# Kernel tuning notes

Measured on AMD Instinct MI355X. Metric: run time of the kernel, lower is better.

Reference implementation:

```python
import jax, jax.numpy as jnp
import numpy as np

D_MODEL = 1024
N_HEADS = 16
D_K = D_MODEL // N_HEADS
SEQ = 2048
BATCH = 2
THETA = 10000.0


def apply_rope(x, positions, theta):
    # x: [..., h, s, d_k], positions: [s]
    d_k = x.shape[-1]
    inv_freq = 1.0 / (theta ** (jnp.arange(0, d_k, 2, dtype=jnp.float32) / d_k))  # [d_k/2]
    ang = positions.astype(jnp.float32)[:, None] * inv_freq[None, :]  # [s, d_k/2]
    cos, sin = jnp.cos(ang), jnp.sin(ang)
    xe, xo = x[..., 0::2], x[..., 1::2]
    re = xe * cos - xo * sin
    ro = xe * sin + xo * cos
    return jnp.stack([re, ro], axis=-1).reshape(x.shape)


def setup_inputs() -> dict:
    key = jax.random.key(0)
    ks = jax.random.split(key, 7)
    f = lambda k, s: jax.random.normal(k, s, dtype=jnp.float32)
    return {
        "Q": f(ks[0], (BATCH, SEQ, D_MODEL)),
        "K": f(ks[1], (BATCH, SEQ, D_MODEL)),
        "V": f(ks[2], (BATCH, SEQ, D_MODEL)),
        "w_q": f(ks[3], (D_MODEL, D_MODEL)) * 0.02,
        "w_k": f(ks[4], (D_MODEL, D_MODEL)) * 0.02,
        "w_v": f(ks[5], (D_MODEL, D_MODEL)) * 0.02,
        "w_o": f(ks[6], (D_MODEL, D_MODEL)) * 0.02,
        "mask": jnp.tril(jnp.ones((SEQ, SEQ), dtype=bool)),
        "token_positions": jnp.arange(SEQ, dtype=jnp.int32),
    }


def reference(Q, K, V, w_q, w_k, w_v, w_o, mask, token_positions):
    h, d_k = N_HEADS, D_K
    # projections: weight is [h*d_k, d_model], applied as x @ W^T
    def proj(x, w):
        y = jnp.einsum('bsd,ed->bse', x, w)
        b, s, _ = y.shape
        return y.reshape(b, s, h, d_k).transpose(0, 2, 1, 3)  # [b,h,s,d_k]
    q = proj(Q, w_q)
    k = proj(K, w_k)
    v = proj(V, w_v)
    q = apply_rope(q, token_positions, THETA)
    k = apply_rope(k, token_positions, THETA)
    scores = jnp.einsum('bhqd,bhkd->bhqk', q, k) / jnp.sqrt(jnp.float32(d_k))
    scores = jnp.where(mask, scores, -jnp.inf)
    attn = jax.nn.softmax(scores, axis=-1)
    out = jnp.einsum('bhqk,bhkd->bhqd', attn, v)
    b, _, s, _ = out.shape
    out = out.transpose(0, 2, 1, 3).reshape(b, s, h * d_k)
    return jnp.einsum('bse,de->bsd', out, w_o)
```

## Files before the change

### kernel.cpp

```cpp
#include <hip/hip_runtime.h>

#define SEQ 2048
#define BATCH 2
#define DM 1024
#define NH 16
#define DK 64
#define BH (BATCH*NH)

typedef __attribute__((ext_vector_type(8))) short bf16x8;
typedef __attribute__((ext_vector_type(4))) float f32x4;

__device__ __forceinline__ ushort f2bf(float f) {
  union { float f; unsigned u; } v; v.f = f;
  unsigned r = (v.u + 0x7fffu + ((v.u >> 16) & 1u)) >> 16;
  return (ushort)r;
}
__device__ __forceinline__ float bf2f(ushort h) {
  union { unsigned u; float f; } v; v.u = ((unsigned)h) << 16;
  return v.f;
}
__device__ __forceinline__ unsigned cvtpk(float lo, float hi) {
  unsigned r;
  asm("v_cvt_pk_bf16_f32 %0, %1, %2" : "=v"(r) : "v"(lo), "v"(hi));
  return r;
}

#define WAITV4 asm volatile("s_waitcnt vmcnt(4)" ::: "memory")
#define WAITV3 asm volatile("s_waitcnt vmcnt(3)" ::: "memory")
#define WAITV2 asm volatile("s_waitcnt vmcnt(2)" ::: "memory")
#define WAITV0 asm volatile("s_waitcnt vmcnt(0)" ::: "memory")
#define WAITL0 asm volatile("s_waitcnt lgkmcnt(0)" ::: "memory")
#define BARR() __builtin_amdgcn_s_barrier()

struct P4 { const float* p0; const float* p1; const float* p2; const float* p3; };
__global__ void k_castN(P4 in, ushort* __restrict__ out, int n4) {
  const float* src = (blockIdx.z == 0) ? in.p0 : (blockIdx.z == 1) ? in.p1
                    : (blockIdx.z == 2) ? in.p2 : in.p3;
  ushort* dst = out + (size_t)blockIdx.z * (size_t)n4 * 4;
  int i = blockIdx.x * blockDim.x + threadIdx.x;
  int st = gridDim.x * blockDim.x;
  for (; i < n4; i += st) {
    float4 v = reinterpret_cast<const float4*>(src)[i];
    ushort4 o;
    o.x = f2bf(v.x); o.y = f2bf(v.y); o.z = f2bf(v.z); o.w = f2bf(v.w);
    reinterpret_cast<ushort4*>(dst)[i] = o;
  }
}

__global__ void k_rope_tab(float* __restrict__ tab) {
  int id = blockIdx.x * blockDim.x + threadIdx.x;
  if (id >= SEQ * 32) return;
  int s = id >> 5, i = id & 31;
  float inv = powf(10000.f, -(float)i / 32.f);
  float ang = (float)s * inv;
  float sn, cs;
  sincosf(ang, &sn, &cs);
  tab[id * 2] = cs;
  tab[id * 2 + 1] = sn;
}

__device__ __forceinline__ void gll16(const void* g, void* l) {
  __builtin_amdgcn_global_load_lds((const __attribute__((address_space(1))) void*)g,
                                   (__attribute__((address_space(3))) void*)l, 16, 0, 0);
}

#define LOADA(R, kk_) do {                                                     \
    _Pragma("unroll")                                                          \
    for (int i_ = 0; i_ < 2; ++i_) {                                           \
      int row_ = i_ * 64 + (tid >> 2), c_ = (tid & 3) * 8;                     \
      const float4* s_ = (const float4*)(Afp + (size_t)(m0 + row_) * K + (kk_) + c_); \
      R[2 * i_] = s_[0]; R[2 * i_ + 1] = s_[1];                                \
    }                                                                          \
  } while (0)

#define AWRITE(AD, R) do {                                                     \
    _Pragma("unroll")                                                          \
    for (int i_ = 0; i_ < 2; ++i_) {                                           \
      int row_ = i_ * 64 + (tid >> 2), c_ = (tid & 3) * 8;                     \
      uint4 pk_;                                                               \
      pk_.x = cvtpk(R[2 * i_].x, R[2 * i_].y);                                 \
      pk_.y = cvtpk(R[2 * i_].z, R[2 * i_].w);                                 \
      pk_.z = cvtpk(R[2 * i_ + 1].x, R[2 * i_ + 1].y);                         \
      pk_.w = cvtpk(R[2 * i_ + 1].z, R[2 * i_ + 1].w);                         \
      *(uint4*)((AD) + row_ * 32 + c_) = pk_;                                  \
    }                                                                          \
  } while (0)

#define GLLB(BD, kk_) do {                                                     \
    gll16(Bw + (size_t)(n0 + w * 16 + lrow) * K + (kk_) + lcol, (void*)((BD) + w * 512));       \
    gll16(Bw + (size_t)(n0 + 64 + w * 16 + lrow) * K + (kk_) + lcol, (void*)((BD) + 2048 + w * 512)); \
  } while (0)

#define GCOMP(AS_, BS_) do {                                                   \
    bf16x8 af[4], bfr[4];                                                      \
    _Pragma("unroll")                                                          \
    for (int i = 0; i < 4; ++i)                                                \
      af[i] = *(const bf16x8*)((AS_) + (wr * 64 + i * 16 + l15) * 32 + l4 * 8);\
    _Pragma("unroll")                                                          \
    for (int i = 0; i < 4; ++i)                                                \
      bfr[i] = *(const bf16x8*)((BS_) + (wc * 64 + i * 16 + l15) * 32 + l4 * 8);\
    _Pragma("unroll")                                                          \
    for (int mi = 0; mi < 4; ++mi)                                             \
      _Pragma("unroll")                                                        \
      for (int ni = 0; ni < 4; ++ni)                                           \
        acc[mi][ni] = __builtin_amdgcn_mfma_f32_16x16x32_bf16(af[mi], bfr[ni], acc[mi][ni], 0, 0, 0); \
  } while (0)

#define PHASE(CAS, CBS, NAS, NBS, RIN, ROUT, T2OK, t_) do {                    \
    GLLB(NBS, ((t_) + 1) * 32);                                                \
    GCOMP(CAS, CBS);                                                           \
    WAITV2;                                                                    \
    AWRITE(NAS, RIN);                                                          \
    if (T2OK) LOADA(ROUT, ((t_) + 2) * 32);                                    \
    if (T2OK) { WAITV4; } else { WAITV0; }                                     \
    WAITL0; BARR();                                                            \
  } while (0)

__global__ __launch_bounds__(256) void k_gemm_qkv(const float* __restrict__ Qf,
                                                  const float* __restrict__ Kf,
                                                  const float* __restrict__ Vf,
                                                  const ushort* __restrict__ Bw0,
                                                  ushort* __restrict__ qT,
                                                  ushort* __restrict__ kT,
                                                  ushort* __restrict__ vT,
                                                  const float* __restrict__ tab,
                                                  float qscale, int M, int N, int K) {
  const int id = blockIdx.x;
  const int mlo = id & 7, nb = (id >> 3) & 7, mhi = (id >> 6) & 3, z = id >> 8;
  const int m0 = (mhi * 8 + mlo) * 128, n0 = nb * 128;
  const float* Afp = (z == 0) ? Qf : (z == 1) ? Kf : Vf;
  const ushort* Bw = Bw0 + (size_t)z * ((size_t)N * K);
  __shared__ ushort As0[128 * 32], Bs0[128 * 32];
  __shared__ ushort As1[128 * 32], Bs1[128 * 32];
  const int tid = threadIdx.x;
  const int w = tid >> 6, lane = tid & 63;
  const int l15 = lane & 15, l4 = lane >> 4;
  const int wr = w >> 1, wc = w & 1;
  const int lrow = lane >> 2, lcol = (lane & 3) * 8;
  float4 rA[4], rB[4];
  f32x4 acc[4][4] = {};
  LOADA(rA, 0);
  GLLB(Bs0, 0);
  WAITV0;
  AWRITE(As0, rA);
  LOADA(rB, 32);
  WAITL0; BARR();
  for (int t = 0; t < 30; t += 2) {
    PHASE(As0, Bs0, As1, Bs1, rB, rA, 1, t);
    PHASE(As1, Bs1, As0, Bs0, rA, rB, 1, t + 1);
  }
  PHASE(As0, Bs0, As1, Bs1, rB, rA, 0, 30);
  GCOMP(As1, Bs1);
  if (z == 2) {
#pragma unroll
    for (int mi = 0; mi < 4; ++mi)
#pragma unroll
      for (int ni = 0; ni < 4; ++ni) {
        int row = m0 + wr * 64 + mi * 16 + l4 * 4;
        int col = n0 + wc * 64 + ni * 16 + l15;
        int bh2 = (row >> 11) * 16 + (col >> 6);
        int d = col & 63, s = row & (SEQ - 1);
        uint2 pk;
        pk.x = cvtpk(acc[mi][ni][0], acc[mi][ni][1]);
        pk.y = cvtpk(acc[mi][ni][2], acc[mi][ni][3]);
        *(uint2*)(vT + ((size_t)bh2 * 64 + d) * SEQ + s) = pk;
      }
  } else {
    const float scale = (z == 0) ? qscale : 1.0f;
    ushort* T = (z == 0) ? qT : kT;
    const bool odd = (l15 & 1);
#pragma unroll
    for (int mi = 0; mi < 4; ++mi)
#pragma unroll
      for (int ni = 0; ni < 4; ++ni)
#pragma unroll
        for (int r = 0; r < 4; ++r) {
          int row = m0 + wr * 64 + mi * 16 + l4 * 4 + r;
          int col = n0 + wc * 64 + ni * 16 + l15;
          float v = acc[mi][ni][r];
          float pv = __shfl_xor(v, 1);
          int s = row & (SEQ - 1);
          int d = col & 63;
          float2 cs = *(const float2*)(tab + ((size_t)s * 32 + (d >> 1)) * 2);
          float xe = odd ? pv : v, xo = odd ? v : pv;
          float outv = (odd ? (xe * cs.y + xo * cs.x) : (xe * cs.x - xo * cs.y)) * scale;
          int bh2 = (row >> 11) * 16 + (col >> 6);
          T[((size_t)bh2 * SEQ + s) * 64 + d] = f2bf(outv);
        }
  }
}

#define FSTAGE(AD, BD, kk_) do {                                               \
    gll16(A + (size_t)(m0 + srow) * K + (kk_) + scol, (void*)((AD) + w * 512));\
    gll16(Bw + (size_t)(n0 + srow) * K + (kk_) + scol, (void*)((BD) + w * 512));\
    gll16(Bw + (size_t)(n0 + 64 + srow) * K + (kk_) + scol, (void*)((BD) + 2048 + w * 512)); \
  } while (0)

#define FCOMP(AS_, BS_) do {                                                   \
    bf16x8 af[2], bfr[4];                                                      \
    _Pragma("unroll")                                                          \
    for (int i = 0; i < 2; ++i)                                                \
      af[i] = *(const bf16x8*)((AS_) + (wr * 32 + i * 16 + l15) * 32 + l4 * 8);\
    _Pragma("unroll")                                                          \
    for (int i = 0; i < 4; ++i)                                                \
      bfr[i] = *(const bf16x8*)((BS_) + (wc * 64 + i * 16 + l15) * 32 + l4 * 8);\
    _Pragma("unroll")                                                          \
    for (int mi = 0; mi < 2; ++mi)                                             \
      _Pragma("unroll")                                                        \
      for (int ni = 0; ni < 4; ++ni)                                           \
        acc[mi][ni] = __builtin_amdgcn_mfma_f32_16x16x32_bf16(af[mi], bfr[ni], acc[mi][ni], 0, 0, 0); \
  } while (0)

__global__ __launch_bounds__(256) void k_gemm_f(const ushort* __restrict__ A,
                                                const ushort* __restrict__ Bw,
                                                float* __restrict__ C, int M, int N, int K) {
  const int id = blockIdx.x;
  const int mlo = id & 7, nb = (id >> 3) & 7, mhi = id >> 6;
  const int m0 = (mhi * 8 + mlo) * 64, n0 = nb * 128;
  __shared__ ushort As0[64 * 32], Bs0[128 * 32];
  __shared__ ushort As1[64 * 32], Bs1[128 * 32];
  const int tid = threadIdx.x;
  const int w = tid >> 6, lane = tid & 63;
  const int l15 = lane & 15, l4 = lane >> 4;
  const int wr = w >> 1, wc = w & 1;
  const int srow = tid >> 2, scol = (tid & 3) * 8;
  f32x4 acc[2][4] = {};
  FSTAGE(As0, Bs0, 0);
  FSTAGE(As1, Bs1, 32);
  for (int kk = 0; kk < K - 64; kk += 64) {
    WAITV3; BARR();
    FCOMP(As0, Bs0);
    WAITL0; BARR();
    FSTAGE(As0, Bs0, kk + 64);
    WAITV3; BARR();
    FCOMP(As1, Bs1);
    WAITL0; BARR();
    if (kk + 96 < K) FSTAGE(As1, Bs1, kk + 96);
  }
  WAITV3; BARR();
  FCOMP(As0, Bs0);
  WAITV0; BARR();
  FCOMP(As1, Bs1);
#pragma unroll
  for (int mi = 0; mi < 2; ++mi)
#pragma unroll
    for (int ni = 0; ni < 4; ++ni)
#pragma unroll
      for (int r = 0; r < 4; ++r) {
        int row = m0 + wr * 32 + mi * 16 + l4 * 4 + r;
        int col = n0 + wc * 64 + ni * 16 + l15;
        C[(size_t)row * N + col] = acc[mi][ni][r];
      }
}

#define KSTAGE(DST, kt_) do {                                                  \
    const ushort* kb_ = kT + hb + (size_t)(kt_) * 8192;                        \
    _Pragma("unroll")                                                          \
    for (int i_ = 0; i_ < 4; ++i_) {                                           \
      int tt_ = i_ * 256 + tid;                                                \
      int row_ = tt_ >> 3, c_ = (tt_ & 7) ^ (row_ & 7);                        \
      gll16(kb_ + (size_t)row_ * 64 + c_ * 8,                                  \
            (void*)((char*)(DST) + (i_ * 256 + w * 64) * 16));                 \
    }                                                                          \
  } while (0)

#define VSTAGE(DST, kt_) do {                                                  \
    const ushort* vb_ = vT + vbase + (size_t)(kt_) * 128;                      \
    _Pragma("unroll")                                                          \
    for (int i_ = 0; i_ < 4; ++i_) {                                           \
      int tt_ = i_ * 256 + tid;                                                \
      int row_ = tt_ >> 4, c_ = (tt_ & 15) ^ (row_ & 15);                      \
      gll16(vb_ + (size_t)row_ * SEQ + c_ * 8,                                 \
            (void*)((char*)(DST) + (i_ * 256 + w * 64) * 16));                 \
    }                                                                          \
  } while (0)

#define FRK(BASE, row_, cidx)                                                  \
  (*(const bf16x8*)((const char*)(BASE) + (row_) * 128 + ((((cidx) ^ ((row_) & 7)) & 7) * 16)))
#define FRV(BASE, row_, cidx)                                                  \
  (*(const bf16x8*)((const char*)(BASE) + (row_) * 256 + ((((cidx) ^ ((row_) & 15)) & 15) * 16)))

#define SMAX8(P, MRUN, LRUN, ACC) do {                                         \
    float mx = P[0][0];                                                        \
    _Pragma("unroll")                                                          \
    for (int nf = 0; nf < 8; ++nf)                                             \
      _Pragma("unroll")                                                        \
      for (int r = 0; r < 4; ++r) mx = fmaxf(mx, P[nf][r]);                    \
    mx = fmaxf(mx, __shfl_xor(mx, 16));                                        \
    mx = fmaxf(mx, __shfl_xor(mx, 32));                                        \
    if (!__all(mx <= MRUN)) {                                                  \
      const float mn = fmaxf(MRUN, mx);                                        \
      const float so = __builtin_amdgcn_exp2f(MRUN - mn);                      \
      float soq[4];                                                            \
      _Pragma("unroll")                                                        \
      for (int r = 0; r < 4; ++r) soq[r] = __shfl(so, l4 * 4 + r);             \
      _Pragma("unroll")                                                        \
      for (int df = 0; df < 4; ++df)                                           \
        _Pragma("unroll")                                                      \
        for (int r = 0; r < 4; ++r) ACC[df][r] *= soq[r];                      \
      LRUN *= so;                                                              \
      MRUN = mn;                                                               \
    }                                                                          \
    float rs = 0.f;                                                            \
    _Pragma("unroll")                                                          \
    for (int nf = 0; nf < 8; ++nf) {                                           \
      float e0 = __builtin_amdgcn_exp2f(P[nf][0] - MRUN);                      \
      float e1 = __builtin_amdgcn_exp2f(P[nf][1] - MRUN);                      \
      float e2 = __builtin_amdgcn_exp2f(P[nf][2] - MRUN);                      \
      float e3 = __builtin_amdgcn_exp2f(P[nf][3] - MRUN);                      \
      P[nf][0] = e0; P[nf][1] = e1; P[nf][2] = e2; P[nf][3] = e3;              \
      rs += (e0 + e1) + (e2 + e3);                                             \
    }                                                                          \
    LRUN += rs;                                                                \
  } while (0)

#define PVHALF(P, MYP, ACC, VC, H) do {                                        \
    _Pragma("unroll")                                                          \
    for (int i = 0; i < 4; ++i) {                                              \
      uint2 pk;                                                                \
      pk.x = cvtpk(P[(H) * 4 + i][0], P[(H) * 4 + i][1]);                      \
      pk.y = cvtpk(P[(H) * 4 + i][2], P[(H) * 4 + i][3]);                      \
      *(uint2*)((MYP) + ((l15 * 128 + i * 32 + l4 * 8) ^ swz)) = pk;           \
    }                                                                          \
    const bf16x8 pa0 = *(const bf16x8*)((MYP) + ((l15 * 128 + l4 * 16) ^ swz));\
    const bf16x8 pa1 = *(const bf16x8*)((MYP) + ((l15 * 128 + 64 + l4 * 16) ^ swz));\
    _Pragma("unroll")                                                          \
    for (int df = 0; df < 4; ++df) {                                           \
      bf16x8 v0_ = FRV(VC, df * 16 + l15, (H) * 8 + l4);                       \
      bf16x8 v1_ = FRV(VC, df * 16 + l15, (H) * 8 + l4 + 4);                   \
      ACC[df] = __builtin_amdgcn_mfma_f32_16x16x32_bf16(pa0, v0_, ACC[df], 0, 0, 0); \
      ACC[df] = __builtin_amdgcn_mfma_f32_16x16x32_bf16(pa1, v1_, ACC[df], 0, 0, 0); \
    }                                                                          \
  } while (0)

#define STEP(KC, VC, KN, VN, kt_, DIAG, PREF) do {                             \
    if (PREF) { KSTAGE(KN, (kt_) + 1); VSTAGE(VN, (kt_) + 1); }                \
    float p0[8][4], p1[8][4];                                                  \
    _Pragma("unroll")                                                          \
    for (int nf = 0; nf < 8; ++nf) {                                           \
      bf16x8 k0_ = FRK(KC, nf * 16 + l15, l4);                                 \
      bf16x8 k1_ = FRK(KC, nf * 16 + l15, l4 + 4);                             \
      if (!(DIAG) || nf < 4) {                                                 \
        f32x4 z = {0.f, 0.f, 0.f, 0.f};                                        \
        z = __builtin_amdgcn_mfma_f32_16x16x32_bf16(k0_, qb00, z, 0, 0, 0);    \
        z = __builtin_amdgcn_mfma_f32_16x16x32_bf16(k1_, qb01, z, 0, 0, 0);    \
        _Pragma("unroll")                                                      \
        for (int r = 0; r < 4; ++r) {                                          \
          float sc = z[r];                                                     \
          if (DIAG && (nf * 16 + l4 * 4 + r) > (w * 16 + l15)) sc = -INFINITY; \
          p0[nf][r] = sc;                                                      \
        }                                                                      \
      } else {                                                                 \
        _Pragma("unroll")                                                      \
        for (int r = 0; r < 4; ++r) p0[nf][r] = -INFINITY;                     \
      }                                                                        \
      {                                                                        \
        f32x4 z = {0.f, 0.f, 0.f, 0.f};                                        \
        z = __builtin_amdgcn_mfma_f32_16x16x32_bf16(k0_, qb10, z, 0, 0, 0);    \
        z = __builtin_amdgcn_mfma_f32_16x16x32_bf16(k1_, qb11, z, 0, 0, 0);    \
        _Pragma("unroll")                                                      \
        for (int r = 0; r < 4; ++r) {                                          \
          float sc = z[r];                                                     \
          if (DIAG && (nf * 16 + l4 * 4 + r) > (64 + w * 16 + l15)) sc = -INFINITY; \
          p1[nf][r] = sc;                                                      \
        }                                                                      \
      }                                                                        \
    }                                                                          \
    SMAX8(p0, mrun0, lrun0, acc0);                                             \
    SMAX8(p1, mrun1, lrun1, acc1);                                             \
    PVHALF(p0, myP0, acc0, VC, 0);                                             \
    if (!(DIAG)) PVHALF(p0, myP0, acc0, VC, 1);                                \
    PVHALF(p1, myP1, acc1, VC, 0);                                             \
    PVHALF(p1, myP1, acc1, VC, 1);                                             \
    __syncthreads();                                                           \
  } while (0)

__global__ __launch_bounds__(256, 2) void k_flash(const ushort* __restrict__ qT,
                                                  const ushort* __restrict__ kT,
                                                  const ushort* __restrict__ vT,
                                                  ushort* __restrict__ AO) {
  __shared__ ushort Ks[2][128 * 64];
  __shared__ ushort Vs[2][64 * 128];
  __shared__ char Plds[4 * 4096];
  const int l = blockIdx.x;
  const int bh = (l & 7) * 4 + ((l >> 3) & 3);
  const int qt = (SEQ / 128 - 1) - (l >> 5);
  const int tid = threadIdx.x, w = tid >> 6, lane = tid & 63;
  const int l15 = lane & 15, l4 = lane >> 4;
  const size_t hb = (size_t)bh * SEQ * DK;
  const size_t vbase = (size_t)bh * DK * SEQ;
  const int qrow0 = qt * 128 + w * 16;
  const int qrow1 = qrow0 + 64;
  const bf16x8 qb00 = *(const bf16x8*)(qT + hb + (size_t)(qrow0 + l15) * 64 + l4 * 8);
  const bf16x8 qb01 = *(const bf16x8*)(qT + hb + (size_t)(qrow0 + l15) * 64 + 32 + l4 * 8);
  const bf16x8 qb10 = *(const bf16x8*)(qT + hb + (size_t)(qrow1 + l15) * 64 + l4 * 8);
  const bf16x8 qb11 = *(const bf16x8*)(qT + hb + (size_t)(qrow1 + l15) * 64 + 32 + l4 * 8);
  f32x4 acc0[4] = {}, acc1[4] = {};
  float mrun0 = -INFINITY, lrun0 = 0.f, mrun1 = -INFINITY, lrun1 = 0.f;
  char* myP0 = (char*)Plds + w * 4096;
  char* myP1 = myP0 + 2048;
  const int swz = (l15 & 7) << 4;
  ushort* kc = &Ks[0][0]; ushort* vc = &Vs[0][0];
  ushort* kn = &Ks[1][0]; ushort* vn = &Vs[1][0];
  KSTAGE(kc, 0); VSTAGE(vc, 0);
  __syncthreads();
  for (int kt = 0; kt < qt; ++kt) {
    STEP(kc, vc, kn, vn, kt, false, true);
    ushort* t;
    t = kc; kc = kn; kn = t;
    t = vc; vc = vn; vn = t;
  }
  STEP(kc, vc, kn, vn, qt, true, false);
  lrun0 += __shfl_xor(lrun0, 16); lrun0 += __shfl_xor(lrun0, 32);
  lrun1 += __shfl_xor(lrun1, 16); lrun1 += __shfl_xor(lrun1, 32);
  const int b = bh >> 4, h = bh & 15;
  float lq0[4], lq1[4];
#pragma unroll
  for (int r = 0; r < 4; ++r) {
    lq0[r] = __shfl(lrun0, l4 * 4 + r);
    lq1[r] = __shfl(lrun1, l4 * 4 + r);
  }
#pragma unroll
  for (int r = 0; r < 4; ++r) {
    float inv0 = 1.f / lq0[r], inv1 = 1.f / lq1[r];
    int qr0 = qrow0 + l4 * 4 + r, qr1 = qrow1 + l4 * 4 + r;
#pragma unroll
    for (int df = 0; df < 4; ++df) {
      AO[(size_t)(b * SEQ + qr0) * DM + h * 64 + df * 16 + l15] = f2bf(acc0[df][r] * inv0);
      AO[(size_t)(b * SEQ + qr1) * DM + h * 64 + df * 16 + l15] = f2bf(acc1[df][r] * inv1);
    }
  }
}

extern "C" void kernel_launch(void* const* d_in, const int* in_sizes, int n_in,
                              void* d_out, int out_size, void* d_ws, size_t ws_size,
                              hipStream_t stream) {
  const float* Q = (const float*)d_in[0];
  const float* K = (const float*)d_in[1];
  const float* V = (const float*)d_in[2];
  const float* wq = (const float*)d_in[3];
  const float* wk = (const float*)d_in[4];
  const float* wv = (const float*)d_in[5];
  const float* wo = (const float*)d_in[6];
  float* out = (float*)d_out;
  char* ws = (char*)d_ws;

  ushort* qT = (ushort*)(ws + 0);
  ushort* kT = (ushort*)(ws + 8388608);
  ushort* vT = (ushort*)(ws + 16777216);
  ushort* WQ = (ushort*)(ws + 25165824);
  ushort* AO = (ushort*)(ws + 33554432);
  float* TAB = (float*)(ws + 41943040);

  const int NW4 = DM * DM / 4;
  P4 win = {wq, wk, wv, wo};
  k_castN<<<dim3(1024, 1, 4), 256, 0, stream>>>(win, WQ, NW4);
  k_rope_tab<<<(SEQ * 32) / 256, 256, 0, stream>>>(TAB);

  const float QSCALE = 0.125f * 1.4426950408889634f;
  k_gemm_qkv<<<768, 256, 0, stream>>>(Q, K, V, WQ, qT, kT, vT, TAB, QSCALE,
                                      BATCH * SEQ, DM, DM);

  k_flash<<<BH * (SEQ / 128), 256, 0, stream>>>(qT, kT, vT, AO);

  k_gemm_f<<<512, 256, 0, stream>>>(AO, WQ + 3 * DM * DM, out, BATCH * SEQ, DM, DM);
}
```

Before: 120.6 us.

## Stage fp32 A tiles directly into LDS and convert to bf16 at fragment load

In the QKV projection GEMM, the fp32 activation tile no longer goes through registers and a separate convert-and-store pass. It is copied straight into LDS with global_load_lds, using an XOR-swizzled layout, and converted to bf16 when the MFMA fragments are read. The K loop becomes a double-buffered pipeline that uses vmcnt waits and barriers around each compute stage. This frees registers and VALU work on the staging path, but doubles the LDS used for A and repeats the fp32-to-bf16 conversion in each wave that reads the same rows.

```diff
diff --git a/kernel.cpp b/kernel.cpp
--- a/kernel.cpp
+++ b/kernel.cpp
@@ -25,9 +25,8 @@
   return r;
 }
 
-#define WAITV4 asm volatile("s_waitcnt vmcnt(4)" ::: "memory")
+#define WAITV6 asm volatile("s_waitcnt vmcnt(6)" ::: "memory")
 #define WAITV3 asm volatile("s_waitcnt vmcnt(3)" ::: "memory")
-#define WAITV2 asm volatile("s_waitcnt vmcnt(2)" ::: "memory")
 #define WAITV0 asm volatile("s_waitcnt vmcnt(0)" ::: "memory")
 #define WAITL0 asm volatile("s_waitcnt lgkmcnt(0)" ::: "memory")
 #define BARR() __builtin_amdgcn_s_barrier()
@@ -64,29 +63,14 @@
                                    (__attribute__((address_space(3))) void*)l, 16, 0, 0);
 }
 
-#define LOADA(R, kk_) do {                                                     \
-    _Pragma("unroll")                                                          \
-    for (int i_ = 0; i_ < 2; ++i_) {                                           \
-      int row_ = i_ * 64 + (tid >> 2), c_ = (tid & 3) * 8;                     \
-      const float4* s_ = (const float4*)(Afp + (size_t)(m0 + row_) * K + (kk_) + c_); \
-      R[2 * i_] = s_[0]; R[2 * i_ + 1] = s_[1];                                \
-    }                                                                          \
-  } while (0)
-
-#define AWRITE(AD, R) do {                                                     \
-    _Pragma("unroll")                                                          \
-    for (int i_ = 0; i_ < 2; ++i_) {                                           \
-      int row_ = i_ * 64 + (tid >> 2), c_ = (tid & 3) * 8;                     \
-      uint4 pk_;                                                               \
-      pk_.x = cvtpk(R[2 * i_].x, R[2 * i_].y);                                 \
-      pk_.y = cvtpk(R[2 * i_].z, R[2 * i_].w);                                 \
-      pk_.z = cvtpk(R[2 * i_ + 1].x, R[2 * i_ + 1].y);                         \
-      pk_.w = cvtpk(R[2 * i_ + 1].z, R[2 * i_ + 1].w);                         \
-      *(uint4*)((AD) + row_ * 32 + c_) = pk_;                                  \
-    }                                                                          \
-  } while (0)
-
-#define GLLB(BD, kk_) do {                                                     \
+#define GSTAGE(AD, BD, kk_) do {                                               \
+    _Pragma("unroll")                                                          \
+    for (int i_ = 0; i_ < 4; ++i_) {                                           \
+      int tt_ = i_ * 256 + tid;                                                \
+      int row_ = tt_ >> 3, c_ = (tt_ & 7) ^ (row_ & 7);                        \
+      gll16(Afp + (size_t)(m0 + row_) * K + (kk_) + c_ * 4,                    \
+            (void*)((char*)(AD) + (i_ * 256 + w * 64) * 16));                  \
+    }                                                                          \
     gll16(Bw + (size_t)(n0 + w * 16 + lrow) * K + (kk_) + lcol, (void*)((BD) + w * 512));       \
     gll16(Bw + (size_t)(n0 + 64 + w * 16 + lrow) * K + (kk_) + lcol, (void*)((BD) + 2048 + w * 512)); \
   } while (0)
@@ -94,8 +78,17 @@
 #define GCOMP(AS_, BS_) do {                                                   \
     bf16x8 af[4], bfr[4];                                                      \
     _Pragma("unroll")                                                          \
-    for (int i = 0; i < 4; ++i)                                                \
-      af[i] = *(const bf16x8*)((AS_) + (wr * 64 + i * 16 + l15) * 32 + l4 * 8);\
+    for (int i = 0; i < 4; ++i) {                                              \
+      int arow_ = wr * 64 + i * 16 + l15;                                      \
+      float4 u0 = *(const float4*)((const char*)(AS_) + arow_ * 128 +          \
+                                   (((l4 * 2) ^ (arow_ & 7)) * 16));           \
+      float4 u1 = *(const float4*)((const char*)(AS_) + arow_ * 128 +          \
+                                   (((l4 * 2 + 1) ^ (arow_ & 7)) * 16));       \
+      uint4 pk_;                                                               \
+      pk_.x = cvtpk(u0.x, u0.y); pk_.y = cvtpk(u0.z, u0.w);                    \
+      pk_.z = cvtpk(u1.x, u1.y); pk_.w = cvtpk(u1.z, u1.w);                    \
+      af[i] = *(bf16x8*)&pk_;                                                  \
+    }                                                                          \
     _Pragma("unroll")                                                          \
     for (int i = 0; i < 4; ++i)                                                \
       bfr[i] = *(const bf16x8*)((BS_) + (wc * 64 + i * 16 + l15) * 32 + l4 * 8);\
@@ -104,16 +97,6 @@
       _Pragma("unroll")                                                        \
       for (int ni = 0; ni < 4; ++ni)                                           \
         acc[mi][ni] = __builtin_amdgcn_mfma_f32_16x16x32_bf16(af[mi], bfr[ni], acc[mi][ni], 0, 0, 0); \
-  } while (0)
-
-#define PHASE(CAS, CBS, NAS, NBS, RIN, ROUT, T2OK, t_) do {                    \
-    GLLB(NBS, ((t_) + 1) * 32);                                                \
-    GCOMP(CAS, CBS);                                                           \
-    WAITV2;                                                                    \
-    AWRITE(NAS, RIN);                                                          \
-    if (T2OK) LOADA(ROUT, ((t_) + 2) * 32);                                    \
-    if (T2OK) { WAITV4; } else { WAITV0; }                                     \
-    WAITL0; BARR();                                                            \
   } while (0)
 
 __global__ __launch_bounds__(256) void k_gemm_qkv(const float* __restrict__ Qf,
@@ -130,26 +113,29 @@
   const int m0 = (mhi * 8 + mlo) * 128, n0 = nb * 128;
   const float* Afp = (z == 0) ? Qf : (z == 1) ? Kf : Vf;
   const ushort* Bw = Bw0 + (size_t)z * ((size_t)N * K);
-  __shared__ ushort As0[128 * 32], Bs0[128 * 32];
-  __shared__ ushort As1[128 * 32], Bs1[128 * 32];
+  __shared__ float As0[4096], As1[4096];
+  __shared__ ushort Bs0[4096], Bs1[4096];
   const int tid = threadIdx.x;
   const int w = tid >> 6, lane = tid & 63;
   const int l15 = lane & 15, l4 = lane >> 4;
   const int wr = w >> 1, wc = w & 1;
   const int lrow = lane >> 2, lcol = (lane & 3) * 8;
-  float4 rA[4], rB[4];
   f32x4 acc[4][4] = {};
-  LOADA(rA, 0);
-  GLLB(Bs0, 0);
-  WAITV0;
-  AWRITE(As0, rA);
-  LOADA(rB, 32);
-  WAITL0; BARR();
-  for (int t = 0; t < 30; t += 2) {
-    PHASE(As0, Bs0, As1, Bs1, rB, rA, 1, t);
-    PHASE(As1, Bs1, As0, Bs0, rA, rB, 1, t + 1);
-  }
-  PHASE(As0, Bs0, As1, Bs1, rB, rA, 0, 30);
+  GSTAGE(As0, Bs0, 0);
+  GSTAGE(As1, Bs1, 32);
+  for (int kk = 0; kk < K - 64; kk += 64) {
+    WAITV6; BARR();
+    GCOMP(As0, Bs0);
+    WAITL0; BARR();
+    GSTAGE(As0, Bs0, kk + 64);
+    WAITV6; BARR();
+    GCOMP(As1, Bs1);
+    WAITL0; BARR();
+    if (kk + 96 < K) GSTAGE(As1, Bs1, kk + 96);
+  }
+  WAITV6; BARR();
+  GCOMP(As0, Bs0);
+  WAITV0; BARR();
   GCOMP(As1, Bs1);
   if (z == 2) {
 #pragma unroll
```

New measurement: 129.0 us. 7.0% more time.
